# Kernel optimization log

Measured on AMD Instinct MI355X. Metric: run time of the kernel, lower is better.

## Reference

```python
import jax, jax.numpy as jnp
import numpy as np

N = 50000      # nodes
E = 800000     # edges
F_IN = 64      # n_features
H = 128        # graph_hidden_layers
LAT = 128      # latent_size
DH = 1024      # dense_hidden_layers
G = 256        # num graphs in batch
EPS = 1e-5


def setup_inputs() -> dict:
    key = jax.random.key(0)
    ks = jax.random.split(key, 32)
    def rn(k, shape, scale=0.05):
        return jax.random.normal(k, shape, dtype=jnp.float32) * scale
    inp = {
        "x": jax.random.normal(ks[0], (N, F_IN), dtype=jnp.float32),
        "origin": jax.random.normal(ks[1], (G, 3), dtype=jnp.float32),
        "direction": jax.random.normal(ks[2], (G, 3), dtype=jnp.float32),
        "edge_index": jax.random.randint(ks[3], (2, E), 0, N, dtype=jnp.int32),
        "batch": jnp.sort(jax.random.randint(ks[4], (N,), 0, G, dtype=jnp.int32)),
        # GCNConv weights
        "W1": rn(ks[5], (F_IN, H)), "b1": jnp.zeros((H,), jnp.float32),
        "W2": rn(ks[6], (H, H)),    "b2": jnp.zeros((H,), jnp.float32),
        "W3": rn(ks[7], (H, LAT)), "b3": jnp.zeros((LAT,), jnp.float32),
        # BatchNorm affine params
        "g1": jnp.ones((H,), jnp.float32),   "be1": jnp.zeros((H,), jnp.float32),
        "g2": jnp.ones((H,), jnp.float32),   "be2": jnp.zeros((H,), jnp.float32),
        "g3": jnp.ones((LAT,), jnp.float32), "be3": jnp.zeros((LAT,), jnp.float32),
        # Dense head: (LAT+6)->DH, then n_dense_layers=2 of DH->DH, then DH->3
        "Wd0": rn(ks[8], (LAT + 6, DH)), "bd0": jnp.zeros((DH,), jnp.float32),
        "Wd1": rn(ks[9], (DH, DH)),      "bd1": jnp.zeros((DH,), jnp.float32),
        "Wd2": rn(ks[10], (DH, DH)),     "bd2": jnp.zeros((DH,), jnp.float32),
        "Wout": rn(ks[11], (DH, 3)),     "bout": jnp.zeros((3,), jnp.float32),
    }
    return inp


def _gcn_conv(x, W, b, src, dst, deg_inv_sqrt):
    """PyG GCNConv with self-loops: D^{-1/2} (A+I) D^{-1/2} x W + b."""
    xW = x @ W  # [N, out]
    norm = deg_inv_sqrt[src] * deg_inv_sqrt[dst]  # [E]
    msg = xW[src] * norm[:, None]                 # gather + scale
    agg = jax.ops.segment_sum(msg, dst, num_segments=N)
    agg = agg + xW * (deg_inv_sqrt * deg_inv_sqrt)[:, None]  # self-loop term
    return agg + b


def _batchnorm(x, gamma, beta):
    m = jnp.mean(x, axis=0)
    v = jnp.mean(jnp.square(x - m), axis=0)
    return (x - m) * jax.lax.rsqrt(v + EPS) * gamma + beta


def reference(x, origin, direction, edge_index, batch,
              W1, b1, W2, b2, W3, b3,
              g1, be1, g2, be2, g3, be3,
              Wd0, bd0, Wd1, bd1, Wd2, bd2, Wout, bout):
    src, dst = edge_index[0], edge_index[1]
    # degree with self-loops (in-degree at dst, matching gcn_norm)
    deg = jax.ops.segment_sum(jnp.ones((E,), jnp.float32), dst, num_segments=N) + 1.0
    deg_inv_sqrt = jax.lax.rsqrt(deg)

    h = jax.nn.relu(_batchnorm(_gcn_conv(x, W1, b1, src, dst, deg_inv_sqrt), g1, be1))
    h = jax.nn.relu(_batchnorm(_gcn_conv(h, W2, b2, src, dst, deg_inv_sqrt), g2, be2))
    h = _batchnorm(_gcn_conv(h, W3, b3, src, dst, deg_inv_sqrt), g3, be3)

    # global mean pool over graphs
    sums = jax.ops.segment_sum(h, batch, num_segments=G)
    cnt = jax.ops.segment_sum(jnp.ones((N,), jnp.float32), batch, num_segments=G)
    pooled = sums / jnp.maximum(cnt, 1.0)[:, None]  # [G, LAT]

    z = jnp.concatenate([pooled, origin, direction], axis=1)  # [G, LAT+6]
    z = jax.nn.relu(z @ Wd0 + bd0)
    z = jax.nn.relu(z @ Wd1 + bd1)
    z = jax.nn.relu(z @ Wd2 + bd2)
    return z @ Wout + bout  # [G, 3]
```

## Files before the change

kernel.cpp:

```cpp
#include <hip/hip_runtime.h>

#define HC 128
#define FIN 64
#define DHID 1024
#define ZK 134
#define ZKP 160

typedef __attribute__((ext_vector_type(8))) short short8;
typedef __attribute__((ext_vector_type(8))) __bf16 bf16x8;
typedef __attribute__((ext_vector_type(4))) float f32x4;
typedef __attribute__((ext_vector_type(8))) unsigned short u16x8;
typedef __attribute__((ext_vector_type(4))) unsigned short u16x4;

union FragU { short8 s; bf16x8 b; u16x8 u; };

__device__ inline unsigned short rne_bf16(float x) {
    union { float f; unsigned u; } v; v.f = x;
    unsigned u = v.u;
    unsigned r = (u + 0x7fffu + ((u >> 16) & 1u)) >> 16;
    return (unsigned short)r;
}
__device__ inline float bf16_to_f(unsigned short h) {
    union { unsigned u; float f; } v; v.u = ((unsigned)h) << 16;
    return v.f;
}

__global__ void k_zero_i(int* p, int n) {
    int i = blockIdx.x * blockDim.x + threadIdx.x;
    if (i < n) p[i] = 0;
}

__global__ void k_deg_i(const int* __restrict__ dst, int* __restrict__ cnt, int E) {
    int i = blockIdx.x * blockDim.x + threadIdx.x;
    if (i < E) atomicAdd(&cnt[dst[i]], 1);
}

__global__ void k_xtobf(const float* __restrict__ x, unsigned short* __restrict__ xb, int n4) {
    int i = blockIdx.x * blockDim.x + threadIdx.x;
    if (i >= n4) return;
    float4 v = ((const float4*)x)[i];
    u16x4 o;
    o[0] = rne_bf16(v.x); o[1] = rne_bf16(v.y);
    o[2] = rne_bf16(v.z); o[3] = rne_bf16(v.w);
    ((u16x4*)xb)[i] = o;
}

__global__ void k_scan1(const int* __restrict__ cnt, int* __restrict__ part,
                        int* __restrict__ bsum, float* __restrict__ dinv, int N) {
    __shared__ int sh[256];
    int t = threadIdx.x, i = blockIdx.x * 256 + t;
    int v = (i < N) ? cnt[i] : 0;
    if (i < N) dinv[i] = rsqrtf((float)v + 1.0f);
    sh[t] = v; __syncthreads();
    #pragma unroll
    for (int off = 1; off < 256; off <<= 1) {
        int tv = (t >= off) ? sh[t - off] : 0;
        __syncthreads();
        sh[t] += tv;
        __syncthreads();
    }
    if (i < N) part[i] = sh[t] - v;
    if (t == 255) bsum[blockIdx.x] = sh[255];
}

__global__ void k_scan2(int* __restrict__ bsum, int nb) {
    __shared__ int sh[256];
    int t = threadIdx.x;
    int v = (t < nb) ? bsum[t] : 0;
    sh[t] = v; __syncthreads();
    #pragma unroll
    for (int off = 1; off < 256; off <<= 1) {
        int tv = (t >= off) ? sh[t - off] : 0;
        __syncthreads();
        sh[t] += tv;
        __syncthreads();
    }
    if (t < nb) bsum[t] = sh[t] - v;
}

__global__ void k_scan3(const int* __restrict__ part, const int* __restrict__ bsum,
                        int* __restrict__ row_start, int* __restrict__ cur, int N) {
    int i = blockIdx.x * 256 + threadIdx.x;
    if (i < N) { row_start[i] = part[i] + bsum[blockIdx.x]; cur[i] = 0; }
}

__global__ void k_scatter(const int* __restrict__ src, const int* __restrict__ dst,
                          const float* __restrict__ dinv, const int* __restrict__ row_start,
                          int* __restrict__ cur, int2* __restrict__ csr, int E) {
    int e = blockIdx.x * blockDim.x + threadIdx.x;
    if (e >= E) return;
    int s = src[e], d = dst[e];
    int pos = row_start[d] + atomicAdd(&cur[d], 1);
    int2 pk; pk.x = s; pk.y = __float_as_int(dinv[s] * dinv[d]);
    csr[pos] = pk;
}

template <int RF> struct BVec;
template <> struct BVec<64>  { using T = u16x4; static const int VPL = 4; };
template <> struct BVec<128> { using T = u16x8; static const int VPL = 8; };

template <int RF>
__global__ __launch_bounds__(256) void k_gather2b(const unsigned short* __restrict__ T,
                                                  const int2* __restrict__ csr,
                                                  const int* __restrict__ row_start,
                                                  const int* __restrict__ cnt,
                                                  const float* __restrict__ dinv,
                                                  unsigned short* __restrict__ agg, int N) {
    using vec = typename BVec<RF>::T;
    constexpr int VPL = BVec<RF>::VPL;
    int tid = threadIdx.x;
    int node = blockIdx.x * 16 + (tid >> 4);
    int q = tid & 15;
    if (node >= N) return;
    int beg = row_start[node];
    int end = beg + cnt[node];
    float d = dinv[node];
    vec sv = ((const vec*)(T + (size_t)node * RF))[q];
    float acc[VPL];
    #pragma unroll
    for (int i = 0; i < VPL; ++i) acc[i] = bf16_to_f(sv[i]) * d * d;
    int j = beg;
    for (; j + 8 <= end; j += 8) {
        int2 e[8];
        #pragma unroll
        for (int u = 0; u < 8; ++u) e[u] = csr[j + u];
        vec v[8];
        #pragma unroll
        for (int u = 0; u < 8; ++u) v[u] = ((const vec*)(T + (size_t)e[u].x * RF))[q];
        #pragma unroll
        for (int u = 0; u < 8; ++u) {
            float nn = __int_as_float(e[u].y);
            #pragma unroll
            for (int i = 0; i < VPL; ++i) acc[i] += bf16_to_f(v[u][i]) * nn;
        }
    }
    for (; j + 2 <= end; j += 2) {
        int2 e0 = csr[j], e1 = csr[j + 1];
        vec v0 = ((const vec*)(T + (size_t)e0.x * RF))[q];
        vec v1 = ((const vec*)(T + (size_t)e1.x * RF))[q];
        float n0 = __int_as_float(e0.y), n1 = __int_as_float(e1.y);
        #pragma unroll
        for (int i = 0; i < VPL; ++i)
            acc[i] += bf16_to_f(v0[i]) * n0 + bf16_to_f(v1[i]) * n1;
    }
    if (j < end) {
        int2 e0 = csr[j];
        vec v0 = ((const vec*)(T + (size_t)e0.x * RF))[q];
        float n0 = __int_as_float(e0.y);
        #pragma unroll
        for (int i = 0; i < VPL; ++i) acc[i] += bf16_to_f(v0[i]) * n0;
    }
    vec o;
    #pragma unroll
    for (int i = 0; i < VPL; ++i) o[i] = rne_bf16(acc[i]);
    ((vec*)(agg + (size_t)node * RF))[q] = o;
}

__global__ void k_bn_reduce(const unsigned short* __restrict__ x, float* __restrict__ stat, int N) {
    int f = threadIdx.x & (HC - 1);
    int half = threadIdx.x >> 7;
    int rpb = (N + gridDim.x - 1) / gridDim.x;
    int r0 = blockIdx.x * rpb;
    int r1 = min(N, r0 + rpb);
    float s = 0.f, ss = 0.f;
    for (int r = r0 + half; r < r1; r += 2) {
        float v = bf16_to_f(x[(size_t)r * HC + f]);
        s += v; ss += v * v;
    }
    __shared__ float sh[256], shq[256];
    sh[threadIdx.x] = s; shq[threadIdx.x] = ss;
    __syncthreads();
    if (half == 0) {
        atomicAdd(&stat[f],      sh[threadIdx.x] + sh[threadIdx.x + HC]);
        atomicAdd(&stat[HC + f], shq[threadIdx.x] + shq[threadIdx.x + HC]);
    }
}

__global__ void k_bn_stats2(const float* __restrict__ stat, const float* __restrict__ gam,
                            const float* __restrict__ bet, float invN,
                            float* __restrict__ scale, float* __restrict__ shift) {
    int f = threadIdx.x;
    float m = stat[f] * invN;
    float var = stat[HC + f] * invN - m * m;
    float istd = rsqrtf(var + 1e-5f);
    float sc = gam[f] * istd;
    scale[f] = sc;
    shift[f] = bet[f] - m * sc;
}

__global__ void k_bn_apply2(unsigned short* __restrict__ t, const float* __restrict__ scale,
                            const float* __restrict__ shift, int total8) {
    int i = blockIdx.x * blockDim.x + threadIdx.x;
    if (i >= total8) return;
    int k0 = (i * 8) & (HC - 1);
    u16x8 v = ((const u16x8*)t)[i];
    u16x8 o;
    #pragma unroll
    for (int j = 0; j < 8; ++j) {
        float f = bf16_to_f(v[j]) * scale[k0 + j] + shift[k0 + j];
        o[j] = rne_bf16(fmaxf(f, 0.f));
    }
    ((u16x8*)t)[i] = o;
}

__global__ void k_pool(const unsigned short* __restrict__ h, const int* __restrict__ batch,
                       const float* __restrict__ stat, const float* __restrict__ gam,
                       const float* __restrict__ bet, float invN,
                       float* __restrict__ pooled, float* __restrict__ cnt, int N) {
    int t = threadIdx.x;
    float m = stat[t] * invN;
    float var = stat[HC + t] * invN - m * m;
    float istd = rsqrtf(var + 1e-5f);
    float scv = gam[t] * istd;
    float shv = bet[t] - m * scv;
    int rpb = (N + gridDim.x - 1) / gridDim.x;
    int r0 = blockIdx.x * rpb;
    int r1 = min(N, r0 + rpb);
    if (r0 >= r1) return;
    int curb = batch[r0];
    float acc = 0.f; float c = 0.f;
    for (int r = r0; r < r1; ++r) {
        int b = batch[r];
        if (b != curb) {
            atomicAdd(&pooled[curb * HC + t], acc);
            if (t == 0) atomicAdd(&cnt[curb], c);
            curb = b; acc = 0.f; c = 0.f;
        }
        acc += bf16_to_f(h[(size_t)r * HC + t]) * scv + shv;
        c += 1.f;
    }
    atomicAdd(&pooled[curb * HC + t], acc);
    if (t == 0) atomicAdd(&cnt[curb], c);
}

__global__ void k_build_z(const float* __restrict__ pooled, const float* __restrict__ cnt,
                          const float* __restrict__ origin, const float* __restrict__ dir,
                          float* __restrict__ z, int G) {
    int g = blockIdx.x;
    int t = threadIdx.x;
    if (t >= ZKP) return;
    float v = 0.f;
    if (t < HC) {
        float c = fmaxf(cnt[g], 1.0f);
        v = pooled[g * HC + t] / c;
    } else if (t < HC + 3) {
        v = origin[g * 3 + (t - HC)];
    } else if (t < HC + 6) {
        v = dir[g * 3 + (t - HC - 3)];
    }
    z[g * ZKP + t] = v;
}

__global__ void k_wprep_all(const float* __restrict__ W1, const float* __restrict__ W2,
                            const float* __restrict__ W3,
                            unsigned short* __restrict__ w1h, unsigned short* __restrict__ w1l,
                            unsigned short* __restrict__ w2h, unsigned short* __restrict__ w2l,
                            unsigned short* __restrict__ w3h, unsigned short* __restrict__ w3l) {
    int i = blockIdx.x * blockDim.x + threadIdx.x;
    const float* W; unsigned short *th, *tl; int K, idx;
    if (i < FIN * HC)           { W = W1; th = w1h; tl = w1l; K = FIN; idx = i; }
    else if (i < FIN*HC + HC*HC){ W = W2; th = w2h; tl = w2l; K = HC;  idx = i - FIN*HC; }
    else if (i < FIN*HC + 2*HC*HC){ W = W3; th = w3h; tl = w3l; K = HC; idx = i - FIN*HC - HC*HC; }
    else return;
    int k = idx >> 7, n = idx & (HC - 1);
    float w = W[idx];
    unsigned short h = rne_bf16(w);
    th[n * K + k] = h;
    tl[n * K + k] = rne_bf16(w - bf16_to_f(h));
}

__global__ __launch_bounds__(256) void k_wprep2(const float* __restrict__ W,
                                                unsigned short* __restrict__ th,
                                                unsigned short* __restrict__ tl,
                                                int K, int KP, int NC) {
    __shared__ float tile[32][33];
    int kt = blockIdx.x * 32, nt = blockIdx.y * 32;
    int tx = threadIdx.x & 31, ty0 = threadIdx.x >> 5;
    #pragma unroll
    for (int i = 0; i < 4; ++i) {
        int ty = ty0 + i * 8;
        int k = kt + ty;
        float v = (k < K) ? W[(size_t)k * NC + nt + tx] : 0.f;
        tile[ty][tx] = v;
    }
    __syncthreads();
    #pragma unroll
    for (int i = 0; i < 4; ++i) {
        int ty = ty0 + i * 8;
        int n = nt + ty;
        int k = kt + tx;
        float w = tile[tx][ty];
        unsigned short h = rne_bf16(w);
        th[(size_t)n * KP + k] = h;
        tl[(size_t)n * KP + k] = rne_bf16(w - bf16_to_f(h));
    }
}

template <int KK>
__global__ __launch_bounds__(512) void gemm_node2(const unsigned short* __restrict__ A,
                                                  const unsigned short* __restrict__ wth,
                                                  const unsigned short* __restrict__ wtl,
                                                  unsigned short* __restrict__ C, int M) {
    constexpr int KS = KK / 32;
    int tid = threadIdx.x;
    int lane = tid & 63, wid = tid >> 6;
    int rw = wid & 1, cg = wid >> 1;
    int l15 = lane & 15, l4 = lane >> 4;
    int cbase = cg * 32;

    FragU bh[2][KS], bl[2][KS];
    #pragma unroll
    for (int ct = 0; ct < 2; ++ct) {
        int n = cbase + ct * 16 + l15;
        #pragma unroll
        for (int ks = 0; ks < KS; ++ks) {
            int k = ks * 32 + l4 * 8;
            bh[ct][ks].s = *(const short8*)(wth + (size_t)n * KK + k);
            bl[ct][ks].s = *(const short8*)(wtl + (size_t)n * KK + k);
        }
    }

    #pragma unroll
    for (int rt = 0; rt < 2; ++rt) {
        int m0 = blockIdx.x * 64 + rt * 32 + rw * 16;
        if (m0 < M) {
            int arow = min(m0 + l15, M - 1);
            f32x4 zero = {0.f, 0.f, 0.f, 0.f};
            f32x4 acc[2] = {zero, zero};
            #pragma unroll
            for (int ks = 0; ks < KS; ++ks) {
                int k0 = ks * 32 + l4 * 8;
                FragU a;
                a.u = *(const u16x8*)(A + (size_t)arow * KK + k0);
                #pragma unroll
                for (int ct = 0; ct < 2; ++ct) {
                    acc[ct] = __builtin_amdgcn_mfma_f32_16x16x32_bf16(a.b, bh[ct][ks].b, acc[ct], 0, 0, 0);
                    acc[ct] = __builtin_amdgcn_mfma_f32_16x16x32_bf16(a.b, bl[ct][ks].b, acc[ct], 0, 0, 0);
                }
            }
            #pragma unroll
            for (int ct = 0; ct < 2; ++ct) {
                int col = cbase + ct * 16 + l15;
                #pragma unroll
                for (int r = 0; r < 4; ++r) {
                    int row = m0 + l4 * 4 + r;
                    if (row < M)
                        C[(size_t)row * HC + col] = rne_bf16(acc[ct][r]);
                }
            }
        }
    }
}

__global__ __launch_bounds__(256) void gemm_head_sk(const float* __restrict__ A,
                                                    const unsigned short* __restrict__ wth,
                                                    const unsigned short* __restrict__ wtl,
                                                    float* __restrict__ Cpart,
                                                    int M, int N, int K, int slice) {
    int tid = threadIdx.x;
    int lane = tid & 63, wid = tid >> 6;
    int rw = wid & 1, cw = wid >> 1;
    int l15 = lane & 15, l4 = lane >> 4;
    int m0 = blockIdx.y * 32 + rw * 16;
    int cb = blockIdx.x * 64 + cw * 32;
    int z = blockIdx.z;
    int kbeg = z * slice;
    int kend = min(K, kbeg + slice);
    if (m0 >= M) return;

    int arow = m0 + l15;
    f32x4 zero = {0.f, 0.f, 0.f, 0.f};
    f32x4 acc[2] = {zero, zero};

    for (int k0 = kbeg; k0 < kend; k0 += 32) {
        int ka = k0 + l4 * 8;
        const float4 p0 = *(const float4*)(A + (size_t)arow * K + ka);
        const float4 p1 = *(const float4*)(A + (size_t)arow * K + ka + 4);
        float av[8] = {p0.x, p0.y, p0.z, p0.w, p1.x, p1.y, p1.z, p1.w};
        FragU ah, al;
        #pragma unroll
        for (int i = 0; i < 8; ++i) {
            unsigned short h = rne_bf16(av[i]);
            ah.s[i] = (short)h;
            al.s[i] = (short)rne_bf16(av[i] - bf16_to_f(h));
        }
        #pragma unroll
        for (int ct = 0; ct < 2; ++ct) {
            int n = cb + ct * 16 + l15;
            FragU bh, bl;
            bh.s = *(const short8*)(wth + (size_t)n * K + ka);
            bl.s = *(const short8*)(wtl + (size_t)n * K + ka);
            acc[ct] = __builtin_amdgcn_mfma_f32_16x16x32_bf16(ah.b, bh.b, acc[ct], 0, 0, 0);
            acc[ct] = __builtin_amdgcn_mfma_f32_16x16x32_bf16(ah.b, bl.b, acc[ct], 0, 0, 0);
            acc[ct] = __builtin_amdgcn_mfma_f32_16x16x32_bf16(al.b, bh.b, acc[ct], 0, 0, 0);
        }
    }

    float* Cz = Cpart + (size_t)z * M * N;
    #pragma unroll
    for (int ct = 0; ct < 2; ++ct) {
        int col = cb + ct * 16 + l15;
        #pragma unroll
        for (int r = 0; r < 4; ++r) {
            int row = m0 + l4 * 4 + r;
            Cz[(size_t)row * N + col] = acc[ct][r];
        }
    }
}

__global__ void k_reduce_br(const float* __restrict__ part, const float* __restrict__ bias,
                            float* __restrict__ C, int MN, int Nmask, int NZ) {
    int i = (blockIdx.x * blockDim.x + threadIdx.x) * 4;
    if (i >= MN) return;
    float4 acc = *(const float4*)(part + i);
    for (int zz = 1; zz < NZ; ++zz) {
        float4 p = *(const float4*)(part + (size_t)zz * MN + i);
        acc.x += p.x; acc.y += p.y; acc.z += p.z; acc.w += p.w;
    }
    int n = i & Nmask;
    acc.x += bias[n]; acc.y += bias[n + 1]; acc.z += bias[n + 2]; acc.w += bias[n + 3];
    acc.x = fmaxf(acc.x, 0.f); acc.y = fmaxf(acc.y, 0.f);
    acc.z = fmaxf(acc.z, 0.f); acc.w = fmaxf(acc.w, 0.f);
    *(float4*)(C + i) = acc;
}

__global__ void k_dense_out(const float* __restrict__ z, const float* __restrict__ W,
                            const float* __restrict__ b, float* __restrict__ out, int K) {
    int g = blockIdx.x;
    const float* zr = z + (size_t)g * K;
    float a0 = 0.f, a1 = 0.f, a2 = 0.f;
    for (int k = threadIdx.x; k < K; k += blockDim.x) {
        float zv = zr[k];
        a0 += zv * W[k * 3 + 0];
        a1 += zv * W[k * 3 + 1];
        a2 += zv * W[k * 3 + 2];
    }
    __shared__ float s[768];
    s[threadIdx.x] = a0; s[256 + threadIdx.x] = a1; s[512 + threadIdx.x] = a2;
    __syncthreads();
    for (int off = 128; off > 0; off >>= 1) {
        if ((int)threadIdx.x < off) {
            s[threadIdx.x]       += s[threadIdx.x + off];
            s[256 + threadIdx.x] += s[256 + threadIdx.x + off];
            s[512 + threadIdx.x] += s[512 + threadIdx.x + off];
        }
        __syncthreads();
    }
    if (threadIdx.x == 0) {
        out[g * 3 + 0] = s[0]   + b[0];
        out[g * 3 + 1] = s[256] + b[1];
        out[g * 3 + 2] = s[512] + b[2];
    }
}

extern "C" void kernel_launch(void* const* d_in, const int* in_sizes, int n_in,
                              void* d_out, int out_size, void* d_ws, size_t ws_size,
                              hipStream_t stream) {
    const float* x         = (const float*)d_in[0];
    const float* origin    = (const float*)d_in[1];
    const float* direction = (const float*)d_in[2];
    const int*   eidx      = (const int*)d_in[3];
    const int*   batch     = (const int*)d_in[4];
    const float* W1 = (const float*)d_in[5];
    const float* W2 = (const float*)d_in[7];
    const float* W3 = (const float*)d_in[9];
    const float* g1 = (const float*)d_in[11]; const float* be1 = (const float*)d_in[12];
    const float* g2 = (const float*)d_in[13]; const float* be2 = (const float*)d_in[14];
    const float* g3 = (const float*)d_in[15]; const float* be3 = (const float*)d_in[16];
    const float* Wd0 = (const float*)d_in[17]; const float* bd0 = (const float*)d_in[18];
    const float* Wd1 = (const float*)d_in[19]; const float* bd1 = (const float*)d_in[20];
    const float* Wd2 = (const float*)d_in[21]; const float* bd2 = (const float*)d_in[22];
    const float* Wout = (const float*)d_in[23]; const float* bout = (const float*)d_in[24];
    float* out = (float*)d_out;

    const int N = in_sizes[4];
    const int E = in_sizes[3] / 2;
    const int G = in_sizes[1] / 3;
    const int* src = eidx;
    const int* dst = eidx + E;

    char* ws = (char*)d_ws;
    size_t off = 0;
    auto alloc = [&](size_t nbytes) -> void* {
        void* p = (void*)(ws + off);
        off += (nbytes + 255) & ~(size_t)255;
        return p;
    };
    float* colstats = (float*)alloc(3 * 2 * HC * 4);
    float* pooled   = (float*)alloc((size_t)G * HC * 4);
    float* cntf     = (float*)alloc((size_t)G * 4);
    const size_t zeroBytes = 3 * 2 * HC * 4 + (size_t)G * HC * 4 + (size_t)G * 4;

    float* dinv     = (float*)alloc((size_t)N * 4);
    int*   degcnt   = (int*)alloc((size_t)N * 4);
    int*   part     = (int*)alloc((size_t)N * 4);
    int*   bsum     = (int*)alloc(256 * 4);
    int*   row_start= (int*)alloc((size_t)N * 4);
    int*   cur      = (int*)alloc((size_t)N * 4);
    int2*  csr      = (int2*)alloc((size_t)E * 8);
    unsigned short* xb   = (unsigned short*)alloc((size_t)N * FIN * 2);
    unsigned short* aggx = (unsigned short*)alloc((size_t)N * FIN * 2);
    unsigned short* tabA = (unsigned short*)alloc((size_t)N * HC * 2);
    unsigned short* tabB = (unsigned short*)alloc((size_t)N * HC * 2);
    unsigned short* wt1h = (unsigned short*)alloc((size_t)FIN * HC * 2);
    unsigned short* wt1l = (unsigned short*)alloc((size_t)FIN * HC * 2);
    unsigned short* wt2h = (unsigned short*)alloc((size_t)HC * HC * 2);
    unsigned short* wt2l = (unsigned short*)alloc((size_t)HC * HC * 2);
    unsigned short* wt3h = (unsigned short*)alloc((size_t)HC * HC * 2);
    unsigned short* wt3l = (unsigned short*)alloc((size_t)HC * HC * 2);
    unsigned short* wd0h = (unsigned short*)alloc((size_t)DHID * ZKP * 2);
    unsigned short* wd0l = (unsigned short*)alloc((size_t)DHID * ZKP * 2);
    unsigned short* wd1h = (unsigned short*)alloc((size_t)DHID * DHID * 2);
    unsigned short* wd1l = (unsigned short*)alloc((size_t)DHID * DHID * 2);
    unsigned short* wd2h = (unsigned short*)alloc((size_t)DHID * DHID * 2);
    unsigned short* wd2l = (unsigned short*)alloc((size_t)DHID * DHID * 2);
    float* bnscale  = (float*)alloc(HC * 4);
    float* bnshift  = (float*)alloc(HC * 4);
    float* zbuf     = (float*)alloc((size_t)G * ZKP * 4);
    float* t0       = (float*)alloc((size_t)G * DHID * 4);
    float* t1       = (float*)alloc((size_t)G * DHID * 4);
    float* kpart    = (float*)alloc((size_t)8 * G * DHID * 4);
    (void)ws_size;

    const int nScanBlk = (N + 255) / 256;
    const int gemmBlk = (N + 63) / 64;
    const int gatherBlk = (N + 15) / 16;
    const int total8 = N * HC / 8;
    const float invN = 1.0f / (float)N;

    hipMemsetAsync(colstats, 0, zeroBytes, stream);

    k_xtobf<<<(N * FIN / 4 + 255) / 256, 256, 0, stream>>>(x, xb, N * FIN / 4);
    k_wprep_all<<<(FIN * HC + 2 * HC * HC + 255) / 256, 256, 0, stream>>>(
        W1, W2, W3, wt1h, wt1l, wt2h, wt2l, wt3h, wt3l);
    k_wprep2<<<dim3(ZKP / 32, DHID / 32), 256, 0, stream>>>(Wd0, wd0h, wd0l, ZK, ZKP, DHID);
    k_wprep2<<<dim3(DHID / 32, DHID / 32), 256, 0, stream>>>(Wd1, wd1h, wd1l, DHID, DHID, DHID);
    k_wprep2<<<dim3(DHID / 32, DHID / 32), 256, 0, stream>>>(Wd2, wd2h, wd2l, DHID, DHID, DHID);

    k_zero_i<<<nScanBlk, 256, 0, stream>>>(degcnt, N);
    k_deg_i<<<(E + 255) / 256, 256, 0, stream>>>(dst, degcnt, E);
    k_scan1<<<nScanBlk, 256, 0, stream>>>(degcnt, part, bsum, dinv, N);
    k_scan2<<<1, 256, 0, stream>>>(bsum, nScanBlk);
    k_scan3<<<nScanBlk, 256, 0, stream>>>(part, bsum, row_start, cur, N);
    k_scatter<<<(E + 255) / 256, 256, 0, stream>>>(src, dst, dinv, row_start, cur, csr, E);

    k_gather2b<FIN><<<gatherBlk, 256, 0, stream>>>(xb, csr, row_start, degcnt, dinv, aggx, N);
    gemm_node2<FIN><<<gemmBlk, 512, 0, stream>>>(aggx, wt1h, wt1l, tabA, N);
    k_bn_reduce<<<256, 256, 0, stream>>>(tabA, colstats + 0 * 2 * HC, N);

    k_bn_stats2<<<1, HC, 0, stream>>>(colstats + 0 * 2 * HC, g1, be1, invN, bnscale, bnshift);
    k_bn_apply2<<<(total8 + 255) / 256, 256, 0, stream>>>(tabA, bnscale, bnshift, total8);
    gemm_node2<HC><<<gemmBlk, 512, 0, stream>>>(tabA, wt2h, wt2l, tabB, N);
    k_gather2b<HC><<<gatherBlk, 256, 0, stream>>>(tabB, csr, row_start, degcnt, dinv, tabA, N);
    k_bn_reduce<<<256, 256, 0, stream>>>(tabA, colstats + 1 * 2 * HC, N);

    k_bn_stats2<<<1, HC, 0, stream>>>(colstats + 1 * 2 * HC, g2, be2, invN, bnscale, bnshift);
    k_bn_apply2<<<(total8 + 255) / 256, 256, 0, stream>>>(tabA, bnscale, bnshift, total8);
    gemm_node2<HC><<<gemmBlk, 512, 0, stream>>>(tabA, wt3h, wt3l, tabB, N);
    k_gather2b<HC><<<gatherBlk, 256, 0, stream>>>(tabB, csr, row_start, degcnt, dinv, tabA, N);
    k_bn_reduce<<<256, 256, 0, stream>>>(tabA, colstats + 2 * 2 * HC, N);

    k_pool<<<512, HC, 0, stream>>>(tabA, batch, colstats + 2 * 2 * HC, g3, be3, invN,
                                   pooled, cntf, N);
    k_build_z<<<G, 192, 0, stream>>>(pooled, cntf, origin, direction, zbuf, G);

    const int MN = G * DHID;
    const int rblk = (MN / 4 + 255) / 256;

    gemm_head_sk<<<dim3(DHID / 64, (G + 31) / 32, 5), 256, 0, stream>>>(
        zbuf, wd0h, wd0l, kpart, G, DHID, ZKP, 32);
    k_reduce_br<<<rblk, 256, 0, stream>>>(kpart, bd0, t0, MN, DHID - 1, 5);

    gemm_head_sk<<<dim3(DHID / 64, (G + 31) / 32, 8), 256, 0, stream>>>(
        t0, wd1h, wd1l, kpart, G, DHID, DHID, 128);
    k_reduce_br<<<rblk, 256, 0, stream>>>(kpart, bd1, t1, MN, DHID - 1, 8);

    gemm_head_sk<<<dim3(DHID / 64, (G + 31) / 32, 8), 256, 0, stream>>>(
        t1, wd2h, wd2l, kpart, G, DHID, DHID, 128);
    k_reduce_br<<<rblk, 256, 0, stream>>>(kpart, bd2, t0, MN, DHID - 1, 8);

    k_dense_out<<<G, 256, 0, stream>>>(t0, Wout, bout, out, DHID);
}
```

Before: 451.7 us.

## Vectorize BN reduce, fuse BN stats into apply, partition CSR scatter by dst range

Several independent changes. The BN column reduction now reads 8 bf16 values per thread with 16-byte loads and uses a shared-memory tree reduction. The separate BN-stats kernel is folded into the apply kernel, which recomputes scale and shift per element, and the degree-count zeroing is merged into the initial memset. The CSR scatter is split into 4 dst-range passes over the edge list, with cur pre-initialised to row_start, to improve atomic and write locality at the cost of reading dst four times.

Result: slower. 536.2 us (+18.7%).

```diff
diff --git a/kernel.cpp b/kernel.cpp
--- a/kernel.cpp
+++ b/kernel.cpp
@@ -5,6 +5,7 @@
 #define DHID 1024
 #define ZK 134
 #define ZKP 160
+#define NSCAT 4
 
 typedef __attribute__((ext_vector_type(8))) short short8;
 typedef __attribute__((ext_vector_type(8))) __bf16 bf16x8;
@@ -23,11 +24,6 @@
 __device__ inline float bf16_to_f(unsigned short h) {
     union { unsigned u; float f; } v; v.u = ((unsigned)h) << 16;
     return v.f;
-}
-
-__global__ void k_zero_i(int* p, int n) {
-    int i = blockIdx.x * blockDim.x + threadIdx.x;
-    if (i < n) p[i] = 0;
 }
 
 __global__ void k_deg_i(const int* __restrict__ dst, int* __restrict__ cnt, int E) {
@@ -81,16 +77,20 @@
 __global__ void k_scan3(const int* __restrict__ part, const int* __restrict__ bsum,
                         int* __restrict__ row_start, int* __restrict__ cur, int N) {
     int i = blockIdx.x * 256 + threadIdx.x;
-    if (i < N) { row_start[i] = part[i] + bsum[blockIdx.x]; cur[i] = 0; }
-}
-
-__global__ void k_scatter(const int* __restrict__ src, const int* __restrict__ dst,
-                          const float* __restrict__ dinv, const int* __restrict__ row_start,
-                          int* __restrict__ cur, int2* __restrict__ csr, int E) {
+    if (i < N) { int v = part[i] + bsum[blockIdx.x]; row_start[i] = v; cur[i] = v; }
+}
+
+__global__ void k_scatter2(const int* __restrict__ src, const int* __restrict__ dst,
+                           const float* __restrict__ dinv,
+                           int* __restrict__ cur, int2* __restrict__ csr,
+                           int E, int rangeSize) {
     int e = blockIdx.x * blockDim.x + threadIdx.x;
     if (e >= E) return;
-    int s = src[e], d = dst[e];
-    int pos = row_start[d] + atomicAdd(&cur[d], 1);
+    int d = dst[e];
+    int lo = blockIdx.y * rangeSize;
+    if (d < lo || d >= lo + rangeSize) return;
+    int s = src[e];
+    int pos = atomicAdd(&cur[d], 1);
     int2 pk; pk.x = s; pk.y = __float_as_int(dinv[s] * dinv[d]);
     csr[pos] = pk;
 }
@@ -156,40 +156,47 @@
     ((vec*)(agg + (size_t)node * RF))[q] = o;
 }
 
-__global__ void k_bn_reduce(const unsigned short* __restrict__ x, float* __restrict__ stat, int N) {
-    int f = threadIdx.x & (HC - 1);
-    int half = threadIdx.x >> 7;
+__global__ __launch_bounds__(256) void k_bn_reduce2(const unsigned short* __restrict__ x,
+                                                    float* __restrict__ stat, int N) {
+    int cg = threadIdx.x & 15;
+    int rr = threadIdx.x >> 4;
     int rpb = (N + gridDim.x - 1) / gridDim.x;
     int r0 = blockIdx.x * rpb;
     int r1 = min(N, r0 + rpb);
-    float s = 0.f, ss = 0.f;
-    for (int r = r0 + half; r < r1; r += 2) {
-        float v = bf16_to_f(x[(size_t)r * HC + f]);
-        s += v; ss += v * v;
-    }
-    __shared__ float sh[256], shq[256];
-    sh[threadIdx.x] = s; shq[threadIdx.x] = ss;
+    float s[8] = {}, ss[8] = {};
+    for (int r = r0 + rr; r < r1; r += 16) {
+        u16x8 v = *(const u16x8*)(x + (size_t)r * HC + cg * 8);
+        #pragma unroll
+        for (int j = 0; j < 8; ++j) { float f = bf16_to_f(v[j]); s[j] += f; ss[j] += f * f; }
+    }
+    __shared__ float shs[16][16][8];
+    __shared__ float shq[16][16][8];
+    #pragma unroll
+    for (int j = 0; j < 8; ++j) { shs[rr][cg][j] = s[j]; shq[rr][cg][j] = ss[j]; }
     __syncthreads();
-    if (half == 0) {
-        atomicAdd(&stat[f],      sh[threadIdx.x] + sh[threadIdx.x + HC]);
-        atomicAdd(&stat[HC + f], shq[threadIdx.x] + shq[threadIdx.x + HC]);
-    }
-}
-
-__global__ void k_bn_stats2(const float* __restrict__ stat, const float* __restrict__ gam,
-                            const float* __restrict__ bet, float invN,
-                            float* __restrict__ scale, float* __restrict__ shift) {
-    int f = threadIdx.x;
-    float m = stat[f] * invN;
-    float var = stat[HC + f] * invN - m * m;
-    float istd = rsqrtf(var + 1e-5f);
-    float sc = gam[f] * istd;
-    scale[f] = sc;
-    shift[f] = bet[f] - m * sc;
-}
-
-__global__ void k_bn_apply2(unsigned short* __restrict__ t, const float* __restrict__ scale,
-                            const float* __restrict__ shift, int total8) {
+    #pragma unroll
+    for (int off = 8; off > 0; off >>= 1) {
+        if (rr < off) {
+            #pragma unroll
+            for (int j = 0; j < 8; ++j) {
+                shs[rr][cg][j] += shs[rr + off][cg][j];
+                shq[rr][cg][j] += shq[rr + off][cg][j];
+            }
+        }
+        __syncthreads();
+    }
+    if (rr == 0) {
+        #pragma unroll
+        for (int j = 0; j < 8; ++j) {
+            atomicAdd(&stat[cg * 8 + j],      shs[0][cg][j]);
+            atomicAdd(&stat[HC + cg * 8 + j], shq[0][cg][j]);
+        }
+    }
+}
+
+__global__ void k_bn_apply3(unsigned short* __restrict__ t, const float* __restrict__ stat,
+                            const float* __restrict__ gam, const float* __restrict__ bet,
+                            float invN, int total8) {
     int i = blockIdx.x * blockDim.x + threadIdx.x;
     if (i >= total8) return;
     int k0 = (i * 8) & (HC - 1);
@@ -197,8 +204,13 @@
     u16x8 o;
     #pragma unroll
     for (int j = 0; j < 8; ++j) {
-        float f = bf16_to_f(v[j]) * scale[k0 + j] + shift[k0 + j];
-        o[j] = rne_bf16(fmaxf(f, 0.f));
+        int k = k0 + j;
+        float m = stat[k] * invN;
+        float var = stat[HC + k] * invN - m * m;
+        float istd = rsqrtf(var + 1e-5f);
+        float sc = gam[k] * istd;
+        float sh = bet[k] - m * sc;
+        o[j] = rne_bf16(fmaxf(bf16_to_f(v[j]) * sc + sh, 0.f));
     }
     ((u16x8*)t)[i] = o;
 }
@@ -489,10 +501,10 @@
     float* colstats = (float*)alloc(3 * 2 * HC * 4);
     float* pooled   = (float*)alloc((size_t)G * HC * 4);
     float* cntf     = (float*)alloc((size_t)G * 4);
-    const size_t zeroBytes = 3 * 2 * HC * 4 + (size_t)G * HC * 4 + (size_t)G * 4;
+    int*   degcnt   = (int*)alloc((size_t)N * 4);
+    const size_t zeroBytes = 3 * 2 * HC * 4 + (size_t)G * HC * 4 + 1024  + (size_t)N * 4;
 
     float* dinv     = (float*)alloc((size_t)N * 4);
-    int*   degcnt   = (int*)alloc((size_t)N * 4);
     int*   part     = (int*)alloc((size_t)N * 4);
     int*   bsum     = (int*)alloc(256 * 4);
     int*   row_start= (int*)alloc((size_t)N * 4);
@@ -514,8 +526,6 @@
     unsigned short* wd1l = (unsigned short*)alloc((size_t)DHID * DHID * 2);
     unsigned short* wd2h = (unsigned short*)alloc((size_t)DHID * DHID * 2);
     unsigned short* wd2l = (unsigned short*)alloc((size_t)DHID * DHID * 2);
-    float* bnscale  = (float*)alloc(HC * 4);
-    float* bnshift  = (float*)alloc(HC * 4);
     float* zbuf     = (float*)alloc((size_t)G * ZKP * 4);
     float* t0       = (float*)alloc((size_t)G * DHID * 4);
     float* t1       = (float*)alloc((size_t)G * DHID * 4);
@@ -527,6 +537,7 @@
     const int gatherBlk = (N + 15) / 16;
     const int total8 = N * HC / 8;
     const float invN = 1.0f / (float)N;
+    const int rangeSize = (N + NSCAT - 1) / NSCAT;
 
     hipMemsetAsync(colstats, 0, zeroBytes, stream);
 
@@ -537,28 +548,28 @@
     k_wprep2<<<dim3(DHID / 32, DHID / 32), 256, 0, stream>>>(Wd1, wd1h, wd1l, DHID, DHID, DHID);
     k_wprep2<<<dim3(DHID / 32, DHID / 32), 256, 0, stream>>>(Wd2, wd2h, wd2l, DHID, DHID, DHID);
 
-    k_zero_i<<<nScanBlk, 256, 0, stream>>>(degcnt, N);
     k_deg_i<<<(E + 255) / 256, 256, 0, stream>>>(dst, degcnt, E);
     k_scan1<<<nScanBlk, 256, 0, stream>>>(degcnt, part, bsum, dinv, N);
     k_scan2<<<1, 256, 0, stream>>>(bsum, nScanBlk);
     k_scan3<<<nScanBlk, 256, 0, stream>>>(part, bsum, row_start, cur, N);
-    k_scatter<<<(E + 255) / 256, 256, 0, stream>>>(src, dst, dinv, row_start, cur, csr, E);
+    k_scatter2<<<dim3((E + 255) / 256, NSCAT), 256, 0, stream>>>(src, dst, dinv, cur, csr,
+                                                                 E, rangeSize);
 
     k_gather2b<FIN><<<gatherBlk, 256, 0, stream>>>(xb, csr, row_start, degcnt, dinv, aggx, N);
     gemm_node2<FIN><<<gemmBlk, 512, 0, stream>>>(aggx, wt1h, wt1l, tabA, N);
-    k_bn_reduce<<<256, 256, 0, stream>>>(tabA, colstats + 0 * 2 * HC, N);
-
-    k_bn_stats2<<<1, HC, 0, stream>>>(colstats + 0 * 2 * HC, g1, be1, invN, bnscale, bnshift);
-    k_bn_apply2<<<(total8 + 255) / 256, 256, 0, stream>>>(tabA, bnscale, bnshift, total8);
+    k_bn_reduce2<<<256, 256, 0, stream>>>(tabA, colstats + 0 * 2 * HC, N);
+
+    k_bn_apply3<<<(total8 + 255) / 256, 256, 0, stream>>>(tabA, colstats + 0 * 2 * HC,
+                                                          g1, be1, invN, total8);
     gemm_node2<HC><<<gemmBlk, 512, 0, stream>>>(tabA, wt2h, wt2l, tabB, N);
     k_gather2b<HC><<<gatherBlk, 256, 0, stream>>>(tabB, csr, row_start, degcnt, dinv, tabA, N);
-    k_bn_reduce<<<256, 256, 0, stream>>>(tabA, colstats + 1 * 2 * HC, N);
-
-    k_bn_stats2<<<1, HC, 0, stream>>>(colstats + 1 * 2 * HC, g2, be2, invN, bnscale, bnshift);
-    k_bn_apply2<<<(total8 + 255) / 256, 256, 0, stream>>>(tabA, bnscale, bnshift, total8);
+    k_bn_reduce2<<<256, 256, 0, stream>>>(tabA, colstats + 1 * 2 * HC, N);
+
+    k_bn_apply3<<<(total8 + 255) / 256, 256, 0, stream>>>(tabA, colstats + 1 * 2 * HC,
+                                                          g2, be2, invN, total8);
     gemm_node2<HC><<<gemmBlk, 512, 0, stream>>>(tabA, wt3h, wt3l, tabB, N);
     k_gather2b<HC><<<gatherBlk, 256, 0, stream>>>(tabB, csr, row_start, degcnt, dinv, tabA, N);
-    k_bn_reduce<<<256, 256, 0, stream>>>(tabA, colstats + 2 * 2 * HC, N);
+    k_bn_reduce2<<<256, 256, 0, stream>>>(tabA, colstats + 2 * 2 * HC, N);
 
     k_pool<<<512, HC, 0, stream>>>(tabA, batch, colstats + 2 * 2 * HC, g3, be3, invN,
                                    pooled, cntf, N);
```
